# Kernel tuning notes

Hardware: AMD Instinct MI355X
Metric: run time of the kernel (lower is better)

Reference implementation:

```python
import jax, jax.numpy as jnp
import numpy as np

# HiLo config: dim=384, num_heads=12, alpha=0.5, window_size=2, qkv_bias=False
DIM = 384
N_HEADS = 12
HEAD_DIM = DIM // N_HEADS            # 32
L_HEADS = int(N_HEADS * 0.5)         # 6
H_HEADS = N_HEADS - L_HEADS          # 6
L_DIM = L_HEADS * HEAD_DIM           # 192
H_DIM = H_HEADS * HEAD_DIM           # 192
WS = 2
SCALE = HEAD_DIM ** -0.5
B, H, W = 2, 96, 96


def setup_inputs() -> dict:
    key = jax.random.key(0)
    ks = jax.random.split(key, 8)
    s = 0.02
    return {
        "x": jax.random.normal(ks[0], (B, DIM, H, W), jnp.float32),
        # weights stored [in, out]; linears have no bias except the two proj layers
        "Wh_qkv": jax.random.normal(ks[1], (DIM, H_DIM * 3), jnp.float32) * s,
        "Wh_proj": jax.random.normal(ks[2], (H_DIM, H_DIM), jnp.float32) * s,
        "bh_proj": jnp.zeros((H_DIM,), jnp.float32),
        "Wl_q": jax.random.normal(ks[3], (DIM, L_DIM), jnp.float32) * s,
        "Wl_kv": jax.random.normal(ks[4], (DIM, L_DIM * 2), jnp.float32) * s,
        "Wl_proj": jax.random.normal(ks[5], (L_DIM, L_DIM), jnp.float32) * s,
        "bl_proj": jnp.zeros((L_DIM,), jnp.float32),
    }


def _hifi(x, Wh_qkv, Wh_proj, bh_proj):
    # x: [B, H, W, C] -> windowed local attention over WS x WS windows
    Bx, Hx, Wx, C = x.shape
    hg, wg = Hx // WS, Wx // WS
    G, n = hg * wg, WS * WS
    xw = x.reshape(Bx, hg, WS, wg, WS, C).transpose(0, 1, 3, 2, 4, 5).reshape(Bx, G, n, C)
    qkv = (xw @ Wh_qkv).reshape(Bx, G, n, 3, H_HEADS, HEAD_DIM)
    qkv = qkv.transpose(3, 0, 1, 4, 2, 5)          # [3, B, G, h, n, d]
    q, k, v = qkv[0], qkv[1], qkv[2]
    attn = jnp.einsum('bghnd,bghmd->bghnm', q, k) * SCALE
    attn = jax.nn.softmax(attn, axis=-1)
    out = jnp.einsum('bghnm,bghmd->bghnd', attn, v)  # [B, G, h, n, d]
    out = out.transpose(0, 1, 3, 2, 4).reshape(Bx, hg, wg, WS, WS, H_DIM)
    out = out.transpose(0, 1, 3, 2, 4, 5).reshape(Bx, Hx, Wx, H_DIM)
    return out @ Wh_proj + bh_proj


def _lofi(x, Wl_q, Wl_kv, Wl_proj, bl_proj):
    # x: [B, H, W, C] -> queries from all tokens, K/V from avg-pooled tokens
    Bx, Hx, Wx, C = x.shape
    N = Hx * Wx
    q = (x.reshape(Bx, N, C) @ Wl_q).reshape(Bx, N, L_HEADS, HEAD_DIM).transpose(0, 2, 1, 3)
    # AvgPool2d(WS, WS) on channels-last layout
    xp = x.reshape(Bx, Hx // WS, WS, Wx // WS, WS, C).mean(axis=(2, 4))  # [B, hg, wg, C]
    M = (Hx // WS) * (Wx // WS)
    kv = (xp.reshape(Bx, M, C) @ Wl_kv).reshape(Bx, M, 2, L_HEADS, HEAD_DIM)
    kv = kv.transpose(2, 0, 3, 1, 4)               # [2, B, h, M, d]
    k, v = kv[0], kv[1]
    attn = jnp.einsum('bhnd,bhmd->bhnm', q, k) * SCALE
    attn = jax.nn.softmax(attn, axis=-1)
    out = jnp.einsum('bhnm,bhmd->bhnd', attn, v)   # [B, h, N, d]
    out = out.transpose(0, 2, 1, 3).reshape(Bx, Hx, Wx, L_DIM)
    return out @ Wl_proj + bl_proj


def reference(x, Wh_qkv, Wh_proj, bh_proj, Wl_q, Wl_kv, Wl_proj, bl_proj):
    Bx, C, Hx, Wx = x.shape
    xc = x.transpose(0, 2, 3, 1)                   # [B, H, W, C]
    hi = _hifi(xc, Wh_qkv, Wh_proj, bh_proj)       # [B, H, W, H_DIM]
    lo = _lofi(xc, Wl_q, Wl_kv, Wl_proj, bl_proj)  # [B, H, W, L_DIM]
    out = jnp.concatenate((hi, lo), axis=-1).reshape(Bx, Hx * Wx, C)
    return out.transpose(0, 2, 1).reshape(Bx, C, Hx, Wx)
```

## Files before the change

### kernel.cpp

```cpp
#include <hip/hip_runtime.h>

typedef unsigned short u16;

#define DEV static __device__ __forceinline__

DEV float bf2f(u16 v) { unsigned x = ((unsigned)v) << 16; return __uint_as_float(x); }
DEV u16 f2bf(float f) {
    unsigned x = __float_as_uint(f);
    unsigned r = (x + 0x7fffu + ((x >> 16) & 1u)) >> 16;
    return (u16)r;
}

constexpr int BATCH = 2;
constexpr int CH    = 384;
constexpr int HH    = 96;
constexpr int WW    = 96;
constexpr int NTOK  = HH * WW;
constexpr int GW    = 48;
constexpr int G     = GW * GW;
constexpr int HEADS = 6;
constexpr int NT    = G / 64;
constexpr float SCALE = 0.17677669529663687f;
constexpr float QKSCALE = 0.25503497438034225f;

typedef __attribute__((ext_vector_type(8)))  short short8v;
typedef __attribute__((ext_vector_type(4)))  float f32x4;
typedef __attribute__((ext_vector_type(16))) float f32x16;

DEV f32x4 mfma16(short8v a, short8v b, f32x4 c) {
    return __builtin_amdgcn_mfma_f32_16x16x32_bf16(a, b, c, 0, 0, 0);
}
DEV f32x16 mfma32(short8v a, short8v b, f32x16 c) {
    return __builtin_amdgcn_mfma_f32_32x32x16_bf16(a, b, c, 0, 0, 0);
}

DEV unsigned cvtpk_bf16(float a, float b) {
    unsigned r;
    asm("v_cvt_pk_bf16_f32 %0, %1, %2" : "=v"(r) : "v"(a), "v"(b));
    return r;
}

DEV float exp2fast(float x) {
    float r;
    asm("v_exp_f32 %0, %1" : "=v"(r) : "v"(x));
    return r;
}

DEV float rcpfast(float x) {
    float r;
    asm("v_rcp_f32 %0, %1" : "=v"(r) : "v"(x));
    return r;
}

DEV void permswap(unsigned& a, unsigned& b) {
    asm("v_permlane32_swap_b32 %0, %1" : "+v"(a), "+v"(b));
}

DEV void unpack8(uint4 u, float* f) {
    unsigned a0 = u.x, a1 = u.y, a2 = u.z, a3 = u.w;
    f[0] = bf2f((u16)(a0 & 0xffffu)); f[1] = bf2f((u16)(a0 >> 16));
    f[2] = bf2f((u16)(a1 & 0xffffu)); f[3] = bf2f((u16)(a1 >> 16));
    f[4] = bf2f((u16)(a2 & 0xffffu)); f[5] = bf2f((u16)(a2 >> 16));
    f[6] = bf2f((u16)(a3 & 0xffffu)); f[7] = bf2f((u16)(a3 >> 16));
}

__global__ __launch_bounds__(256) void prep(const float* __restrict__ x,
        const float* __restrict__ W0, const float* __restrict__ W1,
        const float* __restrict__ W2, const float* __restrict__ W3,
        const float* __restrict__ W4,
        u16* __restrict__ xT, u16* __restrict__ xpool,
        u16* __restrict__ D0, u16* __restrict__ D1, u16* __restrict__ D2,
        u16* __restrict__ D3, u16* __restrict__ D4) {
    __shared__ float ts[32][33];
    int tid = threadIdx.x;
    int id = blockIdx.x;
    if (id < 6912) {
        int cx = id % 288, cy = (id / 288) % 12, b = id / 3456;
        int c0 = cx * 32, r0 = cy * 32;
        int row = tid >> 3, cg = tid & 7;
        float4 v = *(const float4*)&x[(size_t)b * CH * NTOK + (size_t)(r0 + row) * NTOK + c0 + cg * 4];
        ts[row][cg * 4 + 0] = v.x; ts[row][cg * 4 + 1] = v.y;
        ts[row][cg * 4 + 2] = v.z; ts[row][cg * 4 + 3] = v.w;
        __syncthreads();
        int cc = tid >> 3, rg = tid & 7;
        uint2 u;
        u.x = (unsigned)f2bf(ts[rg * 4 + 0][cc]) | ((unsigned)f2bf(ts[rg * 4 + 1][cc]) << 16);
        u.y = (unsigned)f2bf(ts[rg * 4 + 2][cc]) | ((unsigned)f2bf(ts[rg * 4 + 3][cc]) << 16);
        *(uint2*)&xT[(size_t)b * NTOK * CH + (size_t)(c0 + cc) * CH + r0 + rg * 4] = u;
    } else if (id < 8640) {
        int t = id - 6912;
        int mx = t % 72, cy = (t / 72) % 12, b = t / 864;
        int m0 = mx * 32, c0 = cy * 32;
        int cc = tid >> 3, mg = tid & 7;
        const float* xb = x + ((size_t)b * CH + c0 + cc) * NTOK;
        #pragma unroll
        for (int i = 0; i < 4; i++) {
            int m = m0 + mg * 4 + i;
            int gy = m / GW, gx = m - gy * GW;
            const float* p = xb + gy * 2 * WW + gx * 2;
            ts[cc][mg * 4 + i] = 0.25f * (p[0] + p[1] + p[WW] + p[WW + 1]);
        }
        __syncthreads();
        int mm = tid >> 3, cg = tid & 7;
        uint2 u;
        u.x = (unsigned)f2bf(ts[cg * 4 + 0][mm]) | ((unsigned)f2bf(ts[cg * 4 + 1][mm]) << 16);
        u.y = (unsigned)f2bf(ts[cg * 4 + 2][mm]) | ((unsigned)f2bf(ts[cg * 4 + 3][mm]) << 16);
        *(uint2*)&xpool[((size_t)b * G + m0 + mm) * CH + c0 + cg * 4] = u;
    } else {
        int wid = id - 8640;
        const float* src; u16* dst; int R, C; float scale; int cx, cy;
        if (wid < 216)      { src = W0; dst = D0; R = 384; C = 576; scale = 1.f;     cx = wid % 18; cy = wid / 18; }
        else if (wid < 288) { src = W1; dst = D1; R = 384; C = 192; scale = QKSCALE; int t = wid - 216; cx = t % 6;  cy = t / 6; }
        else if (wid < 432) { src = W2; dst = D2; R = 384; C = 384; scale = 1.f;     int t = wid - 288; cx = t % 12; cy = t / 12; }
        else if (wid < 468) { src = W3; dst = D3; R = 192; C = 192; scale = 1.f;     int t = wid - 432; cx = t % 6;  cy = t / 6; }
        else                { src = W4; dst = D4; R = 192; C = 192; scale = 1.f;     int t = wid - 468; cx = t % 6;  cy = t / 6; }
        int c0 = cx * 32, r0 = cy * 32;
        int row = tid >> 3, cg = tid & 7;
        float4 v = *(const float4*)&src[(size_t)(r0 + row) * C + c0 + cg * 4];
        ts[row][cg * 4 + 0] = v.x; ts[row][cg * 4 + 1] = v.y;
        ts[row][cg * 4 + 2] = v.z; ts[row][cg * 4 + 3] = v.w;
        __syncthreads();
        int cc = tid >> 3, rg = tid & 7;
        uint2 u;
        u.x = (unsigned)f2bf(scale * ts[rg * 4 + 0][cc]) | ((unsigned)f2bf(scale * ts[rg * 4 + 1][cc]) << 16);
        u.y = (unsigned)f2bf(scale * ts[rg * 4 + 2][cc]) | ((unsigned)f2bf(scale * ts[rg * 4 + 3][cc]) << 16);
        *(uint2*)&dst[(size_t)(c0 + cc) * R + r0 + rg * 4] = u;
    }
}

template<int K>
DEV void gemm64_body(const u16* __restrict__ Pr, const u16* __restrict__ Qr,
                     u16* pt, u16* qt, int tid, f32x4 acc[4]) {
    int w = tid >> 6, lane = tid & 63;
    int l15 = lane & 15, q4 = lane >> 4;
    int lr = tid >> 2, lc = tid & 3;
    const f32x4 zero4 = {0.f, 0.f, 0.f, 0.f};
    acc[0] = zero4; acc[1] = zero4; acc[2] = zero4; acc[3] = zero4;
    uint4 pv = *(const uint4*)&Pr[(size_t)lr * K + lc * 8];
    uint4 qv = *(const uint4*)&Qr[(size_t)lr * K + lc * 8];
    for (int k0 = 0; k0 < K; k0 += 32) {
        __syncthreads();
        *(uint4*)&pt[lr * 40 + lc * 8] = pv;
        *(uint4*)&qt[lr * 40 + lc * 8] = qv;
        if (k0 + 32 < K) {
            pv = *(const uint4*)&Pr[(size_t)lr * K + k0 + 32 + lc * 8];
            qv = *(const uint4*)&Qr[(size_t)lr * K + k0 + 32 + lc * 8];
        }
        __syncthreads();
        short8v pa = *(const short8v*)&pt[(w * 16 + l15) * 40 + q4 * 8];
        #pragma unroll
        for (int qg = 0; qg < 4; qg++) {
            short8v qb = *(const short8v*)&qt[(qg * 16 + l15) * 40 + q4 * 8];
            acc[qg] = mfma16(pa, qb, acc[qg]);
        }
    }
}

__global__ __launch_bounds__(256) void gemm_all(const u16* __restrict__ WT768,
        const u16* __restrict__ xT, const u16* __restrict__ WlkT,
        const u16* __restrict__ WvT, const u16* __restrict__ xpool,
        u16* __restrict__ tokf, u16* __restrict__ kF, u16* __restrict__ vF) {
    __shared__ u16 pt[64 * 40];
    __shared__ u16 qt[64 * 40];
    int tid = threadIdx.x, id = blockIdx.x;
    int w = tid >> 6, lane = tid & 63, l15 = lane & 15, q4 = lane >> 4;
    f32x4 acc[4];
    if (id < 3456) {
        int px = id % 12, qy = (id / 12) % 144, b = id / 1728;
        gemm64_body<CH>(WT768 + (size_t)px * 64 * CH,
                        xT + ((size_t)b * NTOK + qy * 64) * CH, pt, qt, tid, acc);
        #pragma unroll
        for (int qg = 0; qg < 4; qg++) {
            int q = qy * 64 + qg * 16 + l15;
            int p = px * 64 + w * 16 + q4 * 4;
            uint2 pk;
            pk.x = (unsigned)f2bf(acc[qg][0]) | ((unsigned)f2bf(acc[qg][1]) << 16);
            pk.y = (unsigned)f2bf(acc[qg][2]) | ((unsigned)f2bf(acc[qg][3]) << 16);
            *(uint2*)&tokf[((size_t)b * NTOK + q) * 768 + p] = pk;
        }
    } else if (id < 3672) {
        int u = id - 3456;
        int px = u % 3, qy = (u / 3) % 36, b = u / 108;
        gemm64_body<CH>(WlkT + (size_t)px * 64 * CH,
                        xpool + ((size_t)b * G + qy * 64) * CH, pt, qt, tid, acc);
        #pragma unroll
        for (int qg = 0; qg < 4; qg++) {
            int m = qy * 64 + qg * 16 + l15;
            int d = px * 64 + w * 16 + q4 * 4;
            int h = d >> 5, dh = (d >> 4) & 1, hi2 = (d >> 3) & 1;
            int kh = (m >> 5) & 1, tile = m >> 6, slot = kh * 2 + dh;
            int lane2 = (m & 31) + 32 * hi2;
            size_t addr = ((((size_t)(b * HEADS + h) * NT + tile) * 4 + slot) * 64 + lane2) * 8 + (d & 7);
            uint2 pk;
            pk.x = (unsigned)f2bf(acc[qg][0]) | ((unsigned)f2bf(acc[qg][1]) << 16);
            pk.y = (unsigned)f2bf(acc[qg][2]) | ((unsigned)f2bf(acc[qg][3]) << 16);
            *(uint2*)&kF[addr] = pk;
        }
    } else {
        int u = id - 3672;
        int px = u % 36, qy = (u / 36) % 3, b = u / 108;
        gemm64_body<CH>(xpool + ((size_t)b * G + px * 64) * CH,
                        WvT + (size_t)qy * 64 * CH, pt, qt, tid, acc);
        #pragma unroll
        for (int qg = 0; qg < 4; qg++) {
            int jj = qy * 64 + qg * 16 + l15;
            int m = px * 64 + w * 16 + q4 * 4;
            int h = jj >> 5, d31 = jj & 31;
            int tile = m >> 6, slot = (m >> 4) & 3, hi2 = (m >> 3) & 1;
            int lane2 = d31 + 32 * hi2;
            size_t addr = ((((size_t)(b * HEADS + h) * NT + tile) * 4 + slot) * 64 + lane2) * 8 + (m & 7);
            uint2 pk;
            pk.x = (unsigned)f2bf(acc[qg][0]) | ((unsigned)f2bf(acc[qg][1]) << 16);
            pk.y = (unsigned)f2bf(acc[qg][2]) | ((unsigned)f2bf(acc[qg][3]) << 16);
            *(uint2*)&vF[addr] = pk;
        }
    }
}

__global__ __launch_bounds__(256, 4) void mega_attn(const u16* __restrict__ tokf,
        const u16* __restrict__ kF, const u16* __restrict__ vF,
        u16* __restrict__ hi_ao, u16* __restrict__ lo_ao) {
    __shared__ float smem[6528];
    int tid = threadIdx.x;
    int id = blockIdx.x;
    const f32x16 zero16 = {0.f,0.f,0.f,0.f,0.f,0.f,0.f,0.f,0.f,0.f,0.f,0.f,0.f,0.f,0.f,0.f};

    if (id < 3456) {
        int lane = tid & 63, kq = tid >> 6;
        int l31 = lane & 31, hi = lane >> 5;
        int qt = id % 288, h = (id / 288) % HEADS, b = id / 1728;

        const short8v ones = {(short)0x3F80, (short)0x3F80, (short)0x3F80, (short)0x3F80,
                              (short)0x3F80, (short)0x3F80, (short)0x3F80, (short)0x3F80};

        short8v qb0, qb1;
        {
            int nq = qt * 32 + l31;
            const u16* qrow = &tokf[((size_t)b * NTOK + nq) * 768 + 576 + h * 32];
            qb0 = *(const short8v*)&qrow[hi * 8];
            qb1 = *(const short8v*)&qrow[16 + hi * 8];
        }
        f32x16 accO = zero16, accL = zero16;

        const u16* kp = kF + ((size_t)(b * HEADS + h) * NT + kq * 9) * 2048 + lane * 8;
        const u16* vp = vF + ((size_t)(b * HEADS + h) * NT + kq * 9) * 2048 + lane * 8;

        for (int t = 0; t < 9; t++) {
            short8v kb0 = *(const short8v*)(kp);
            short8v kb1 = *(const short8v*)(kp + 512);
            short8v kb2 = *(const short8v*)(kp + 1024);
            short8v kb3 = *(const short8v*)(kp + 1536);
            short8v vb0 = *(const short8v*)(vp);
            short8v vb1 = *(const short8v*)(vp + 512);
            short8v vb2 = *(const short8v*)(vp + 1024);
            short8v vb3 = *(const short8v*)(vp + 1536);
            kp += 2048; vp += 2048;

            f32x16 s0 = mfma32(kb0, qb0, zero16);
            s0 = mfma32(kb1, qb1, s0);
            unsigned pk0[8];
            #pragma unroll
            for (int i = 0; i < 8; i++)
                pk0[i] = cvtpk_bf16(exp2fast(s0[2 * i]), exp2fast(s0[2 * i + 1]));
            permswap(pk0[0], pk0[2]);
            permswap(pk0[1], pk0[3]);
            permswap(pk0[4], pk0[6]);
            permswap(pk0[5], pk0[7]);

            f32x16 s1 = mfma32(kb2, qb0, zero16);
            s1 = mfma32(kb3, qb1, s1);
            unsigned pk1[8];
            #pragma unroll
            for (int i = 0; i < 8; i++)
                pk1[i] = cvtpk_bf16(exp2fast(s1[2 * i]), exp2fast(s1[2 * i + 1]));
            permswap(pk1[0], pk1[2]);
            permswap(pk1[1], pk1[3]);
            permswap(pk1[4], pk1[6]);
            permswap(pk1[5], pk1[7]);

            union { unsigned u[4]; short8v v; } pa;
            pa.u[0] = pk0[0]; pa.u[1] = pk0[1]; pa.u[2] = pk0[2]; pa.u[3] = pk0[3];
            accO = mfma32(pa.v, vb0, accO);
            accL = mfma32(pa.v, ones, accL);
            pa.u[0] = pk0[4]; pa.u[1] = pk0[5]; pa.u[2] = pk0[6]; pa.u[3] = pk0[7];
            accO = mfma32(pa.v, vb1, accO);
            accL = mfma32(pa.v, ones, accL);
            pa.u[0] = pk1[0]; pa.u[1] = pk1[1]; pa.u[2] = pk1[2]; pa.u[3] = pk1[3];
            accO = mfma32(pa.v, vb2, accO);
            accL = mfma32(pa.v, ones, accL);
            pa.u[0] = pk1[4]; pa.u[1] = pk1[5]; pa.u[2] = pk1[6]; pa.u[3] = pk1[7];
            accO = mfma32(pa.v, vb3, accO);
            accL = mfma32(pa.v, ones, accL);
        }

        float* mO = smem;
        float* mL = smem + 3264;
        if (kq) {
            int base = (kq - 1) * 1088 + lane * 17;
            #pragma unroll
            for (int r = 0; r < 16; r++) {
                mO[base + r] = accO[r];
                mL[base + r] = accL[r];
            }
        }
        __syncthreads();
        if (kq == 0) {
            #pragma unroll
            for (int w2 = 0; w2 < 3; w2++) {
                int base = w2 * 1088 + lane * 17;
                #pragma unroll
                for (int r = 0; r < 16; r++) {
                    accO[r] += mO[base + r];
                    accL[r] += mL[base + r];
                }
            }
            #pragma unroll
            for (int r = 0; r < 16; r++) {
                int qr = (r & 3) + 8 * (r >> 2) + 4 * hi;
                int n = qt * 32 + qr;
                lo_ao[((size_t)b * NTOK + n) * 192 + h * 32 + l31] =
                    f2bf(accO[r] * rcpfast(accL[r]));
            }
        }
    } else {
        int bg = id - 3456;
        int b = bg / G, g = bg % G;
        int gy = g / GW, gx = g % GW;
        float (*sq)[576] = (float(*)[576])smem;
        float* satt = smem + 2304;
        float* sp   = smem + 2400;

        for (int c = tid; c < 288; c += 256) {
            int t = c / 72, j8 = c - t * 72;
            int n = (gy * 2 + (t >> 1)) * WW + gx * 2 + (t & 1);
            uint4 u = *(const uint4*)&tokf[((size_t)b * NTOK + n) * 768 + j8 * 8];
            unpack8(u, &sq[t][j8 * 8]);
        }
        __syncthreads();

        if (tid < 96) {
            int h = tid >> 4, tq = (tid >> 2) & 3, tm = tid & 3;
            const float* qp = &sq[tq][h * 32];
            const float* kp = &sq[tm][192 + h * 32];
            float s0 = 0, s1 = 0, s2 = 0, s3 = 0;
            #pragma unroll
            for (int d = 0; d < 32; d += 4) {
                s0 += qp[d] * kp[d];
                s1 += qp[d + 1] * kp[d + 1];
                s2 += qp[d + 2] * kp[d + 2];
                s3 += qp[d + 3] * kp[d + 3];
            }
            satt[h * 16 + tq * 4 + tm] = (s0 + s1 + s2 + s3) * SCALE;
        }
        __syncthreads();
        if (tid < 24) {
            int h = tid >> 2, t = tid & 3;
            float l0 = satt[h * 16 + t * 4 + 0], l1 = satt[h * 16 + t * 4 + 1];
            float l2 = satt[h * 16 + t * 4 + 2], l3 = satt[h * 16 + t * 4 + 3];
            float mx = fmaxf(fmaxf(l0, l1), fmaxf(l2, l3));
            float e0 = __expf(l0 - mx), e1 = __expf(l1 - mx);
            float e2 = __expf(l2 - mx), e3 = __expf(l3 - mx);
            float inv = 1.0f / (e0 + e1 + e2 + e3);
            sp[h * 16 + t * 4 + 0] = e0 * inv; sp[h * 16 + t * 4 + 1] = e1 * inv;
            sp[h * 16 + t * 4 + 2] = e2 * inv; sp[h * 16 + t * 4 + 3] = e3 * inv;
        }
        __syncthreads();
        {
            int t = tid >> 6, hp = (tid >> 5) & 1, d = tid & 31;
            int n = (gy * 2 + (t >> 1)) * WW + gx * 2 + (t & 1);
            u16* op = &hi_ao[((size_t)b * NTOK + n) * 192];
            #pragma unroll
            for (int hh = 0; hh < 3; hh++) {
                int h = hp * 3 + hh;
                float o = sp[h * 16 + t * 4 + 0] * sq[0][384 + h * 32 + d]
                        + sp[h * 16 + t * 4 + 1] * sq[1][384 + h * 32 + d]
                        + sp[h * 16 + t * 4 + 2] * sq[2][384 + h * 32 + d]
                        + sp[h * 16 + t * 4 + 3] * sq[3][384 + h * 32 + d];
                op[h * 32 + d] = f2bf(o);
            }
        }
    }
}

__global__ __launch_bounds__(256) void proj_both(const u16* __restrict__ hi_ao,
        const u16* __restrict__ lo_ao, const u16* __restrict__ WhpT,
        const u16* __restrict__ WlpT, const float* __restrict__ bh,
        const float* __restrict__ bl, float* __restrict__ out) {
    __shared__ u16 pt[64 * 40];
    __shared__ u16 qt[64 * 40];
    int tid = threadIdx.x;
    int z = blockIdx.z, which = z >> 1, b = z & 1;
    const u16* A = which ? lo_ao : hi_ao;
    const u16* W = which ? WlpT : WhpT;
    const float* bias = which ? bl : bh;
    int p0 = blockIdx.x * 64, q0 = blockIdx.y * 64;
    f32x4 acc[4];
    gemm64_body<192>(A + ((size_t)b * NTOK + p0) * 192, W + (size_t)q0 * 192,
                     pt, qt, tid, acc);
    int w = tid >> 6, lane = tid & 63, l15 = lane & 15, q4 = lane >> 4;
    #pragma unroll
    for (int qg = 0; qg < 4; qg++) {
        int q = q0 + qg * 16 + l15;
        int p = p0 + w * 16 + q4 * 4;
        float bb = bias[q];
        float4 o = make_float4(acc[qg][0] + bb, acc[qg][1] + bb,
                               acc[qg][2] + bb, acc[qg][3] + bb);
        *(float4*)&out[((size_t)b * CH + which * 192 + q) * NTOK + p] = o;
    }
}

extern "C" void kernel_launch(void* const* d_in, const int* in_sizes, int n_in,
                              void* d_out, int out_size, void* d_ws, size_t ws_size,
                              hipStream_t stream) {
    const float* x       = (const float*)d_in[0];
    const float* Wh_qkv  = (const float*)d_in[1];
    const float* Wh_proj = (const float*)d_in[2];
    const float* bh_proj = (const float*)d_in[3];
    const float* Wl_q    = (const float*)d_in[4];
    const float* Wl_kv   = (const float*)d_in[5];
    const float* Wl_proj = (const float*)d_in[6];
    const float* bl_proj = (const float*)d_in[7];
    float* out = (float*)d_out;

    char* ws = (char*)d_ws;
    u16*   tokf  = (u16*)ws;
    char*  ws1   = ws + (size_t)28311552;
    u16*   xT    = (u16*)ws1;
    u16*   hi_ao = (u16*)ws1;
    u16*   lo_ao = (u16*)(ws1 + 7077888);
    char*  ws2   = ws1 + (size_t)14155776;
    u16*   kF    = (u16*)ws2;
    u16*   vF    = (u16*)(ws2 + 1769472);
    char*  ws3   = ws2 + (size_t)7077888;
    u16*   xpool = (u16*)ws3;
    char*  ws4   = ws3 + (size_t)3538944;
    u16*   WT768 = (u16*)ws4;
    u16*   WlkvT = WT768 + 768 * 384;
    u16*   WhpT  = WlkvT + 384 * 384;
    u16*   WlpT  = WhpT + 192 * 192;
    u16*   WlkT  = WlkvT;
    u16*   WvT   = WlkvT + 192 * 384;

    prep<<<dim3(9144), 256, 0, stream>>>(
        x, Wh_qkv, Wl_q, Wl_kv, Wh_proj, Wl_proj,
        xT, xpool, WT768, WT768 + 576 * 384, WlkvT, WhpT, WlpT);

    gemm_all<<<dim3(3888), 256, 0, stream>>>(
        WT768, xT, WlkT, WvT, xpool, tokf, kF, vF);

    mega_attn<<<dim3(8064), 256, 0, stream>>>(tokf, kF, vF, hi_ao, lo_ao);

    proj_both<<<dim3(144, 3, 4), 256, 0, stream>>>(
        hi_ao, lo_ao, WhpT, WlpT, bh_proj, bl_proj, out);
}
```

Before: 125.0 us.

## Use 128x128 tiles for main QKV GEMM and interleave attention block types

The large QKV projection in gemm_all moves from 64x64 to 128x128 output tiles with a 4x4 MFMA grid per wave. This raises operand reuse and cuts global-load traffic, at the cost of more registers and fewer blocks. mega_attn now interleaves lofi and hifi blocks in a 3:4 pattern so the two workloads mix across CUs. Its cross-wave reduction stores the row-sum accumulator once per half-wave instead of per lane, which shrinks shared memory and may allow higher occupancy.

```diff
diff --git a/kernel.cpp b/kernel.cpp
--- a/kernel.cpp
+++ b/kernel.cpp
@@ -160,27 +160,72 @@
         const u16* __restrict__ xT, const u16* __restrict__ WlkT,
         const u16* __restrict__ WvT, const u16* __restrict__ xpool,
         u16* __restrict__ tokf, u16* __restrict__ kF, u16* __restrict__ vF) {
-    __shared__ u16 pt[64 * 40];
-    __shared__ u16 qt[64 * 40];
+    __shared__ u16 pt[128 * 40];
+    __shared__ u16 qt[128 * 40];
     int tid = threadIdx.x, id = blockIdx.x;
     int w = tid >> 6, lane = tid & 63, l15 = lane & 15, q4 = lane >> 4;
-    f32x4 acc[4];
-    if (id < 3456) {
-        int px = id % 12, qy = (id / 12) % 144, b = id / 1728;
-        gemm64_body<CH>(WT768 + (size_t)px * 64 * CH,
-                        xT + ((size_t)b * NTOK + qy * 64) * CH, pt, qt, tid, acc);
-        #pragma unroll
-        for (int qg = 0; qg < 4; qg++) {
-            int q = qy * 64 + qg * 16 + l15;
-            int p = px * 64 + w * 16 + q4 * 4;
-            uint2 pk;
-            pk.x = (unsigned)f2bf(acc[qg][0]) | ((unsigned)f2bf(acc[qg][1]) << 16);
-            pk.y = (unsigned)f2bf(acc[qg][2]) | ((unsigned)f2bf(acc[qg][3]) << 16);
-            *(uint2*)&tokf[((size_t)b * NTOK + q) * 768 + p] = pk;
-        }
-    } else if (id < 3672) {
-        int u = id - 3456;
+    const f32x4 zero4 = {0.f, 0.f, 0.f, 0.f};
+    if (id < 864) {
+        int px = id % 6, qy = (id / 6) % 72, b = id / 432;
+        const u16* Pb = WT768 + (size_t)px * 128 * CH;
+        const u16* Qb = xT + ((size_t)b * NTOK + qy * 128) * CH;
+        int wr = (w >> 1) * 64, wc = (w & 1) * 64;
+        f32x4 acc[4][4];
+        #pragma unroll
+        for (int i = 0; i < 4; i++)
+            #pragma unroll
+            for (int j = 0; j < 4; j++) acc[i][j] = zero4;
+        uint4 pv[2], qv[2];
+        #pragma unroll
+        for (int i = 0; i < 2; i++) {
+            int e = tid + i * 256, r = e >> 2, c = e & 3;
+            pv[i] = *(const uint4*)&Pb[(size_t)r * CH + c * 8];
+            qv[i] = *(const uint4*)&Qb[(size_t)r * CH + c * 8];
+        }
+        for (int k0 = 0; k0 < CH; k0 += 32) {
+            __syncthreads();
+            #pragma unroll
+            for (int i = 0; i < 2; i++) {
+                int e = tid + i * 256, r = e >> 2, c = e & 3;
+                *(uint4*)&pt[r * 40 + c * 8] = pv[i];
+                *(uint4*)&qt[r * 40 + c * 8] = qv[i];
+            }
+            if (k0 + 32 < CH) {
+                #pragma unroll
+                for (int i = 0; i < 2; i++) {
+                    int e = tid + i * 256, r = e >> 2, c = e & 3;
+                    pv[i] = *(const uint4*)&Pb[(size_t)r * CH + k0 + 32 + c * 8];
+                    qv[i] = *(const uint4*)&Qb[(size_t)r * CH + k0 + 32 + c * 8];
+                }
+            }
+            __syncthreads();
+            short8v pa[4], qb[4];
+            #pragma unroll
+            for (int i = 0; i < 4; i++) {
+                pa[i] = *(const short8v*)&pt[(wr + i * 16 + l15) * 40 + q4 * 8];
+                qb[i] = *(const short8v*)&qt[(wc + i * 16 + l15) * 40 + q4 * 8];
+            }
+            #pragma unroll
+            for (int i = 0; i < 4; i++)
+                #pragma unroll
+                for (int j = 0; j < 4; j++)
+                    acc[i][j] = mfma16(pa[i], qb[j], acc[i][j]);
+        }
+        #pragma unroll
+        for (int i = 0; i < 4; i++)
+            #pragma unroll
+            for (int j = 0; j < 4; j++) {
+                int p = px * 128 + wr + i * 16 + q4 * 4;
+                int q = qy * 128 + wc + j * 16 + l15;
+                uint2 pk;
+                pk.x = (unsigned)f2bf(acc[i][j][0]) | ((unsigned)f2bf(acc[i][j][1]) << 16);
+                pk.y = (unsigned)f2bf(acc[i][j][2]) | ((unsigned)f2bf(acc[i][j][3]) << 16);
+                *(uint2*)&tokf[((size_t)b * NTOK + q) * 768 + p] = pk;
+            }
+    } else if (id < 1080) {
+        int u = id - 864;
         int px = u % 3, qy = (u / 3) % 36, b = u / 108;
+        f32x4 acc[4];
         gemm64_body<CH>(WlkT + (size_t)px * 64 * CH,
                         xpool + ((size_t)b * G + qy * 64) * CH, pt, qt, tid, acc);
         #pragma unroll
@@ -197,8 +242,9 @@
             *(uint2*)&kF[addr] = pk;
         }
     } else {
-        int u = id - 3672;
+        int u = id - 1080;
         int px = u % 36, qy = (u / 36) % 3, b = u / 108;
+        f32x4 acc[4];
         gemm64_body<CH>(xpool + ((size_t)b * G + px * 64) * CH,
                         WvT + (size_t)qy * 64 * CH, pt, qt, tid, acc);
         #pragma unroll
@@ -220,15 +266,16 @@
 __global__ __launch_bounds__(256, 4) void mega_attn(const u16* __restrict__ tokf,
         const u16* __restrict__ kF, const u16* __restrict__ vF,
         u16* __restrict__ hi_ao, u16* __restrict__ lo_ao) {
-    __shared__ float smem[6528];
+    __shared__ float smem[3168];
     int tid = threadIdx.x;
-    int id = blockIdx.x;
+    int grp = blockIdx.x / 7, rem = blockIdx.x % 7;
     const f32x16 zero16 = {0.f,0.f,0.f,0.f,0.f,0.f,0.f,0.f,0.f,0.f,0.f,0.f,0.f,0.f,0.f,0.f};
 
-    if (id < 3456) {
+    if (rem < 3) {
+        int lid = grp * 3 + rem;
         int lane = tid & 63, kq = tid >> 6;
         int l31 = lane & 31, hi = lane >> 5;
-        int qt = id % 288, h = (id / 288) % HEADS, b = id / 1728;
+        int qt = lid % 288, h = (lid / 288) % HEADS, b = lid / 1728;
 
         const short8v ones = {(short)0x3F80, (short)0x3F80, (short)0x3F80, (short)0x3F80,
                               (short)0x3F80, (short)0x3F80, (short)0x3F80, (short)0x3F80};
@@ -294,24 +341,25 @@
         }
 
         float* mO = smem;
-        float* mL = smem + 3264;
+        float* mL = smem + 3072;
         if (kq) {
-            int base = (kq - 1) * 1088 + lane * 17;
-            #pragma unroll
-            for (int r = 0; r < 16; r++) {
-                mO[base + r] = accO[r];
-                mL[base + r] = accL[r];
+            int base = (kq - 1) * 1024;
+            #pragma unroll
+            for (int r = 0; r < 16; r++) mO[base + r * 64 + lane] = accO[r];
+            if (l31 == 0) {
+                #pragma unroll
+                for (int r = 0; r < 16; r++) mL[(kq - 1) * 32 + hi * 16 + r] = accL[r];
             }
         }
         __syncthreads();
         if (kq == 0) {
             #pragma unroll
             for (int w2 = 0; w2 < 3; w2++) {
-                int base = w2 * 1088 + lane * 17;
+                int base = w2 * 1024;
                 #pragma unroll
                 for (int r = 0; r < 16; r++) {
-                    accO[r] += mO[base + r];
-                    accL[r] += mL[base + r];
+                    accO[r] += mO[base + r * 64 + lane];
+                    accL[r] += mL[w2 * 32 + hi * 16 + r];
                 }
             }
             #pragma unroll
@@ -323,7 +371,7 @@
             }
         }
     } else {
-        int bg = id - 3456;
+        int bg = grp * 4 + (rem - 3);
         int b = bg / G, g = bg % G;
         int gy = g / GW, gx = g % GW;
         float (*sq)[576] = (float(*)[576])smem;
@@ -445,7 +493,7 @@
         x, Wh_qkv, Wl_q, Wl_kv, Wh_proj, Wl_proj,
         xT, xpool, WT768, WT768 + 576 * 384, WlkvT, WhpT, WlpT);
 
-    gemm_all<<<dim3(3888), 256, 0, stream>>>(
+    gemm_all<<<dim3(1296), 256, 0, stream>>>(
         WT768, xT, WlkT, WvT, xpool, tokf, kF, vF);
 
     mega_attn<<<dim3(8064), 256, 0, stream>>>(tokf, kF, vF, hi_ao, lo_ao);
```

Result: slower. 155.9 us (+24.7%).
